# Optimization experiments

Measured on AMD Instinct MI355X. Metric: run time of the kernel, lower is better.

Reference implementation:

```python
import jax, jax.numpy as jnp
import numpy as np
from jax.scipy.linalg import expm

D = 512      # d_model
S = 3        # num_scales
BATCH = 256
H = 8        # attention heads
HD = D // H  # head dim


def layernorm(x, g, b, eps=1e-5):
    m = jnp.mean(x, axis=-1, keepdims=True)
    v = jnp.var(x, axis=-1, keepdims=True)
    return (x - m) / jnp.sqrt(v + eps) * g + b


def setup_inputs() -> dict:
    key = jax.random.key(0)
    ks = jax.random.split(key, 16)
    sd = 1.0 / np.sqrt(D)
    inp = {
        'x': jax.random.normal(ks[0], (BATCH, D), jnp.float32),
        'h_prev': jax.random.normal(ks[1], (BATCH, D), jnp.float32),
        'lstm_h': jax.random.normal(ks[2], (S, BATCH, D), jnp.float32) * 0.1,
        'lstm_c': jax.random.normal(ks[3], (S, BATCH, D), jnp.float32) * 0.1,
        'A': jax.random.normal(ks[4], (D, D), jnp.float32) * sd,
        'Bm': jax.random.normal(ks[5], (D, D), jnp.float32) * sd,
        'dn_w1': jax.random.normal(ks[6], (D, D), jnp.float32) * sd,
        'dn_b1': jnp.zeros((D,), jnp.float32),
        'dn_g': jnp.ones((D,), jnp.float32),
        'dn_beta': jnp.zeros((D,), jnp.float32),
        'dn_w2': jax.random.normal(ks[7], (1, D), jnp.float32) * sd,
        'dn_b2': jnp.zeros((1,), jnp.float32),
        'lstm_wih': jax.random.normal(ks[8], (S, 4 * D, D), jnp.float32) * sd,
        'lstm_whh': jax.random.normal(ks[9], (S, 4 * D, D), jnp.float32) * sd,
        'lstm_bih': jnp.zeros((S, 4 * D), jnp.float32),
        'lstm_bhh': jnp.zeros((S, 4 * D), jnp.float32),
        'decays': jnp.linspace(0.5, 0.95, S, dtype=jnp.float32),
        'attn_in_w': jax.random.normal(ks[10], (3 * D, D), jnp.float32) * sd,
        'attn_in_b': jnp.zeros((3 * D,), jnp.float32),
        'attn_out_w': jax.random.normal(ks[11], (D, D), jnp.float32) * sd,
        'attn_out_b': jnp.zeros((D,), jnp.float32),
        'proj_w': jax.random.normal(ks[12], (D, (S + 2) * D), jnp.float32) * (1.0 / np.sqrt((S + 2) * D)),
        'proj_b': jnp.zeros((D,), jnp.float32),
        'proj_g': jnp.ones((D,), jnp.float32),
        'proj_beta': jnp.zeros((D,), jnp.float32),
    }
    return inp


def reference(x, h_prev, lstm_h, lstm_c, A, Bm, dn_w1, dn_b1, dn_g, dn_beta,
              dn_w2, dn_b2, lstm_wih, lstm_whh, lstm_bih, lstm_bhh, decays,
              attn_in_w, attn_in_b, attn_out_w, attn_out_b,
              proj_w, proj_b, proj_g, proj_beta):
    # ---- delta_net: Linear -> LayerNorm -> GELU(exact) -> Linear -> Softplus ----
    h1 = layernorm(x @ dn_w1.T + dn_b1, dn_g, dn_beta)
    h1 = jax.nn.gelu(h1, approximate=False)
    delta = jax.nn.softplus(h1 @ dn_w2.T + dn_b2)           # (B, 1)

    # ---- SSM update: h_t = expm(delta*A) h_prev + delta*B x ----
    A_disc = jax.vmap(expm)(delta[:, :, None] * A)          # (B, D, D)
    h_ssm = jnp.einsum('bij,bj->bi', A_disc, h_prev) + delta * jnp.einsum('ij,bj->bi', Bm, x)

    # ---- multi-scale LSTM cells (vectorized over scales) ----
    gates = (jnp.einsum('bd,skd->sbk', x, lstm_wih)
             + jnp.einsum('sbd,skd->sbk', lstm_h, lstm_whh)
             + (lstm_bih + lstm_bhh)[:, None, :])           # (S, B, 4D)
    gi, gf, gg, go = jnp.split(gates, 4, axis=-1)
    i_g = jax.nn.sigmoid(gi)
    f_g = jax.nn.sigmoid(gf)
    g_g = jnp.tanh(gg)
    o_g = jax.nn.sigmoid(go)
    c_raw = f_g * lstm_c + i_g * g_g                        # (S, B, D)
    h_new = o_g * jnp.tanh(c_raw)                           # (S, B, D)
    dec = decays[:, None, None]
    c_new = dec * lstm_c + (1.0 - dec) * c_raw              # (S, B, D)

    # ---- fusion attention: 1 query (h_ssm), S keys/values (h_new) ----
    Wq, Wk, Wv = jnp.split(attn_in_w, 3, axis=0)
    bq, bk, bv = jnp.split(attn_in_b, 3, axis=0)
    kv = jnp.transpose(h_new, (1, 0, 2))                    # (B, S, D)
    q = (h_ssm @ Wq.T + bq).reshape(-1, 1, H, HD).transpose(0, 2, 1, 3)   # (B,H,1,HD)
    k = (kv @ Wk.T + bk).reshape(-1, S, H, HD).transpose(0, 2, 1, 3)      # (B,H,S,HD)
    v = (kv @ Wv.T + bv).reshape(-1, S, H, HD).transpose(0, 2, 1, 3)
    scores = jnp.einsum('bhqe,bhke->bhqk', q, k) / np.sqrt(HD)
    attn = jax.nn.softmax(scores, axis=-1)
    ctx = jnp.einsum('bhqk,bhke->bhqe', attn, v)            # (B,H,1,HD)
    ctx = ctx.transpose(0, 2, 1, 3).reshape(-1, D)          # (B, D)
    fused = ctx @ attn_out_w.T + attn_out_b                 # (B, D)

    # ---- output projection over concat [h_ssm, fused, h_1..h_S] ----
    combined = jnp.concatenate([h_ssm, fused] + [h_new[i] for i in range(S)], axis=-1)
    output = layernorm(combined @ proj_w.T + proj_b, proj_g, proj_beta)
    return (output, h_ssm, h_new, c_new)
```

## Files before the change

### kernel.cpp

```cpp
#include <hip/hip_runtime.h>
#include <math.h>

#define DIM 512
#define NB 256
#define KMAX 12

using bf16x8 = __attribute__((ext_vector_type(8))) short;
using f32x4  = __attribute__((ext_vector_type(4))) float;
using float4v = __attribute__((ext_vector_type(4))) float;
using ushort4v = __attribute__((ext_vector_type(4))) unsigned short;

__device__ __forceinline__ unsigned short f2b(float f) {
    union { float f; unsigned int u; } v; v.f = f;
    unsigned int r = v.u + 0x7fffu + ((v.u >> 16) & 1u);
    return (unsigned short)(r >> 16);
}
__device__ __forceinline__ float b2f(unsigned short u) {
    union { unsigned int u; float f; } v; v.u = ((unsigned int)u) << 16;
    return v.f;
}
__device__ __forceinline__ ushort4v f2b4(float4v v) {
    ushort4v o;
    o.x = f2b(v.x); o.y = f2b(v.y); o.z = f2b(v.z); o.w = f2b(v.w);
    return o;
}

__device__ __forceinline__ void block_reduce2(float& s, float& q, float* sb1, float* sb2)
{
    int tid = threadIdx.x;
    #pragma unroll
    for (int off = 32; off > 0; off >>= 1) {
        s += __shfl_down(s, off);
        q += __shfl_down(q, off);
    }
    if ((tid & 63) == 0) { sb1[tid >> 6] = s; sb2[tid >> 6] = q; }
    __syncthreads();
    s = sb1[0] + sb1[1] + sb1[2] + sb1[3];
    q = sb2[0] + sb2[1] + sb2[2] + sb2[3];
    __syncthreads();
}

struct GemmDesc {
    const unsigned short* X;
    const unsigned short* W;
    const float* bias;
    float* Cf;
    unsigned short* Cb;
    unsigned short* Ct;
    int M, N, K, ldX, ldW, ldC, ldCb, tr_row0, acc;
};
struct GemmArgs { GemmDesc d[8]; };
struct LnParams {
    const float* pre; const float* g; const float* beta;
    const float* w2; const float* b2; float* delta; float* coeff;
    int lnd_y;
    const float* cin; const float* bih; const float* bhh; const float* decays;
    float* hout; float* cout; unsigned short* combb;
};

__global__ __launch_bounds__(256) void gemm_mfma(GemmArgs args, LnParams lp)
{
    __shared__ unsigned short lsA[2][8192];
    __shared__ unsigned short lsB[2][8192];
    __shared__ float sb1[4], sb2[4];

    if ((int)blockIdx.y == lp.lnd_y) {
        int b = blockIdx.x, tid = threadIdx.x;
        int i0 = tid, i1 = tid + 256;
        float x0 = lp.pre[(size_t)b * DIM + i0];
        float x1 = lp.pre[(size_t)b * DIM + i1];
        float s = x0 + x1, q = x0 * x0 + x1 * x1;
        block_reduce2(s, q, sb1, sb2);
        float mean = s * (1.f / DIM);
        float var  = q * (1.f / DIM) - mean * mean;
        float inv  = rsqrtf(var + 1e-5f);
        float y0 = (x0 - mean) * inv * lp.g[i0] + lp.beta[i0];
        float y1 = (x1 - mean) * inv * lp.g[i1] + lp.beta[i1];
        float h0 = 0.5f * y0 * (1.f + erff(y0 * 0.70710678118654752f));
        float h1 = 0.5f * y1 * (1.f + erff(y1 * 0.70710678118654752f));
        float p = h0 * lp.w2[i0] + h1 * lp.w2[i1];
        float dummy = 0.f;
        block_reduce2(p, dummy, sb1, sb2);
        if (tid == 0) {
            float z = p + lp.b2[0];
            float d = (z > 20.f) ? z : log1pf(expf(z));
            lp.delta[b] = d;
            float c = 1.f;
            lp.coeff[b] = 1.f;
            for (int k = 1; k <= KMAX; ++k) { c *= d / (float)k; lp.coeff[k * 256 + b] = c; }
        }
        return;
    }

    GemmDesc de = args.d[blockIdx.y];
    int tmm = de.M >> 6;
    int tiles = tmm * (de.N >> 6);
    int t = blockIdx.x;
    if (t >= tiles) return;
    int qc = tiles >> 3, rc = tiles & 7;
    int xcd = t & 7, li = t >> 3;
    int tt = (xcd < rc) ? (xcd * (qc + 1) + li) : (rc * (qc + 1) + (xcd - rc) * qc + li);
    int m0 = (tt % tmm) << 6;
    int n0 = (tt / tmm) << 6;

    int tid = threadIdx.x;
    int w = tid >> 6;
    int l = tid & 63;
    int nkt = de.K >> 7;

    int srow = w * 16 + (l >> 2);
    int schk = l & 3;
    const unsigned short* gA = de.X + (size_t)(m0 + srow) * de.ldX + schk * 8;
    const unsigned short* gB = de.W + (size_t)(n0 + srow) * de.ldW + schk * 8;
    unsigned short* lA = &lsA[0][(w * 64 + l) * 8];
    unsigned short* lB = &lsB[0][(w * 64 + l) * 8];

#define STAGE(bufi, kt)                                                          \
    do {                                                                         \
        for (int hh = 0; hh < 4; ++hh) {                                         \
            __builtin_amdgcn_global_load_lds(                                    \
                (const __attribute__((address_space(1))) unsigned int*)(gA + (size_t)(kt) * 128 + hh * 32), \
                (__attribute__((address_space(3))) unsigned int*)(lA + (bufi) * 8192 + hh * 2048), 16, 0, 0); \
            __builtin_amdgcn_global_load_lds(                                    \
                (const __attribute__((address_space(1))) unsigned int*)(gB + (size_t)(kt) * 128 + hh * 32), \
                (__attribute__((address_space(3))) unsigned int*)(lB + (bufi) * 8192 + hh * 2048), 16, 0, 0); \
        }                                                                        \
    } while (0)

    int mbase = (w >> 1) * 32;
    int nbase = (w & 1) * 32;

    f32x4 acc[2][2];
    #pragma unroll
    for (int i = 0; i < 2; ++i)
        #pragma unroll
        for (int j = 0; j < 2; ++j)
            acc[i][j] = (f32x4){0.f, 0.f, 0.f, 0.f};

    int kg = l >> 4;
    int fr = l & 15;
    int aslot = (mbase * 4 + fr * 4 + kg) * 8;
    int bslot = (nbase * 4 + fr * 4 + kg) * 8;

    STAGE(0, 0);

    for (int kt = 0; kt < nkt; ++kt) {
        __syncthreads();
        if (kt + 1 < nkt) STAGE((kt + 1) & 1, kt + 1);

        const unsigned short* bufA = &lsA[kt & 1][0];
        const unsigned short* bufB = &lsB[kt & 1][0];
        #pragma unroll
        for (int h = 0; h < 4; ++h) {
            bf16x8 a0 = *(const bf16x8*)(bufA + h * 2048 + aslot);
            bf16x8 a1 = *(const bf16x8*)(bufA + h * 2048 + aslot + 512);
            bf16x8 b0 = *(const bf16x8*)(bufB + h * 2048 + bslot);
            bf16x8 b1 = *(const bf16x8*)(bufB + h * 2048 + bslot + 512);
            acc[0][0] = __builtin_amdgcn_mfma_f32_16x16x32_bf16(a0, b0, acc[0][0], 0, 0, 0);
            acc[0][1] = __builtin_amdgcn_mfma_f32_16x16x32_bf16(a0, b1, acc[0][1], 0, 0, 0);
            acc[1][0] = __builtin_amdgcn_mfma_f32_16x16x32_bf16(a1, b0, acc[1][0], 0, 0, 0);
            acc[1][1] = __builtin_amdgcn_mfma_f32_16x16x32_bf16(a1, b1, acc[1][1], 0, 0, 0);
        }
    }

    if (de.acc == 3) {
        __syncthreads();
        float* tile = (float*)lsA;
        #pragma unroll
        for (int mi = 0; mi < 2; ++mi)
            #pragma unroll
            for (int ni = 0; ni < 2; ++ni) {
                int ct = nbase + ni * 16 + fr;
                #pragma unroll
                for (int r = 0; r < 4; ++r) {
                    int rt = mbase + mi * 16 + kg * 4 + r;
                    tile[rt * 65 + ct] = acc[mi][ni][r];
                }
            }
        __syncthreads();
        int s = de.tr_row0;
        int d0 = n0 >> 2;
        float dec = lp.decays[s];
        for (int cell = tid; cell < 1024; cell += 256) {
            int row = cell >> 4, dsub = cell & 15;
            int d = d0 + dsub;
            int b = m0 + row;
            float vgi = tile[row * 65 +      dsub] + lp.bih[s * 2048 +        d] + lp.bhh[s * 2048 +        d];
            float vgf = tile[row * 65 + 16 + dsub] + lp.bih[s * 2048 +  512 + d] + lp.bhh[s * 2048 +  512 + d];
            float vgg = tile[row * 65 + 32 + dsub] + lp.bih[s * 2048 + 1024 + d] + lp.bhh[s * 2048 + 1024 + d];
            float vgo = tile[row * 65 + 48 + dsub] + lp.bih[s * 2048 + 1536 + d] + lp.bhh[s * 2048 + 1536 + d];
            float cc = lp.cin[(size_t)s * 131072 + (size_t)b * 512 + d];
            float ig = 1.f / (1.f + expf(-vgi));
            float fg = 1.f / (1.f + expf(-vgf));
            float g_ = tanhf(vgg);
            float og = 1.f / (1.f + expf(-vgo));
            float craw = fg * cc + ig * g_;
            float hn = og * tanhf(craw);
            lp.hout[(size_t)s * 131072 + (size_t)b * 512 + d] = hn;
            lp.cout[(size_t)s * 131072 + (size_t)b * 512 + d] = dec * cc + (1.f - dec) * craw;
            lp.combb[(size_t)b * 2048 + 512 + s * 512 + d] = f2b(hn);
        }
        return;
    }

    #pragma unroll
    for (int mi = 0; mi < 2; ++mi) {
        #pragma unroll
        for (int ni = 0; ni < 2; ++ni) {
            int col = n0 + nbase + ni * 16 + fr;
            float bv = de.bias ? de.bias[col] : 0.f;
            #pragma unroll
            for (int r = 0; r < 4; ++r) {
                int row = m0 + mbase + mi * 16 + (l >> 4) * 4 + r;
                float v = acc[mi][ni][r] + bv;
                if (de.Cf) {
                    if (de.acc == 2)      atomicAdd(&de.Cf[(size_t)row * de.ldC + col], v);
                    else if (de.acc == 1) de.Cf[(size_t)row * de.ldC + col] += v;
                    else                  de.Cf[(size_t)row * de.ldC + col] = v;
                }
                if (de.Cb)
                    de.Cb[(size_t)row * de.ldCb + col] = f2b(v);
                if (de.Ct && row >= de.tr_row0)
                    de.Ct[(size_t)col * 512 + (row - de.tr_row0)] = f2b(v);
            }
        }
    }
#undef STAGE
}

#define NSEG 13
struct PrepArgs {
    const float* sA[NSEG]; const float* sB[NSEG]; unsigned short* dst[NSEG];
    int n4[NSEG], dRL4[NSEG], sRLA4[NSEG], sRLB4[NSEG], half4[NSEG], offA[NSEG], gmap[NSEG];
    const float* A; unsigned short* ATb;
    const float* W2src; unsigned short* W2dst;
    const float* projw; const float* projb; const float* aoutb; float* pbc;
};
__global__ __launch_bounds__(256) void prep_kernel(PrepArgs a)
{
    __shared__ float tile[32][33];
    int bid = blockIdx.x, tid = threadIdx.x;
    if (bid < 2048) {
        const int gstride = 2048 * 256;
        int g0 = bid * 256 + tid;
        for (int seg = 0; seg < NSEG; ++seg) {
            int n4 = a.n4[seg];
            const float* sA = a.sA[seg];
            const float* sB = a.sB[seg];
            unsigned short* d = a.dst[seg];
            int dRL4 = a.dRL4[seg], sRLA4 = a.sRLA4[seg], sRLB4 = a.sRLB4[seg];
            int half4 = a.half4[seg], offA = a.offA[seg], gm = a.gmap[seg];
            for (int i = g0; i < n4; i += gstride) {
                int r = i / dRL4, c = i - r * dRL4;
                int rs = gm ? (((r >> 4) & 3) * 512 + ((r >> 6) << 4) + (r & 15)) : r;
                const float* src = (c < half4)
                    ? sA + ((size_t)rs * sRLA4 + offA + c) * 4
                    : sB + ((size_t)rs * sRLB4 + (c - half4)) * 4;
                float4v v = *(const float4v*)src;
                *(ushort4v*)(d + (size_t)i * 4) = f2b4(v);
            }
        }
    } else if (bid < 2560) {
        int tt = bid - 2048;
        const float* src = a.A;
        unsigned short* dst = a.ATb;
        if (tt >= 256) { tt -= 256; src = a.W2src; dst = a.W2dst; }
        int bx = tt & 15, by = tt >> 4;
        int tx = tid & 31, ty = tid >> 5;
        #pragma unroll
        for (int i = 0; i < 32; i += 8)
            tile[ty + i][tx] = src[(size_t)(by * 32 + ty + i) * 512 + bx * 32 + tx];
        __syncthreads();
        #pragma unroll
        for (int i = 0; i < 32; i += 8)
            dst[(size_t)(bx * 32 + ty + i) * 512 + by * 32 + tx] = f2b(tile[tx][ty + i]);
    } else {
        int i = (bid - 2560) * 256 + tid;
        const float* pr = a.projw + (size_t)i * 2560 + 512;
        float acc = 0.f;
        for (int j = 0; j < 512; j += 4) {
            float4v w = *(const float4v*)(pr + j);
            float4v ab = *(const float4v*)(a.aoutb + j);
            acc += w.x * ab.x + w.y * ab.y + w.z * ab.z + w.w * ab.w;
        }
        a.pbc[i] = a.projb[i] + acc;
    }
}

__global__ void pointwise_fused(
    const float* __restrict__ Tm, const float* __restrict__ coeff,
    const float* __restrict__ h_prev, const float* __restrict__ delta,
    const float* __restrict__ Bx, float* __restrict__ hssm,
    unsigned short* __restrict__ combb)
{
    int idx4 = blockIdx.x * 256 + threadIdx.x;
    int base = idx4 * 4;
    int b = base >> 9, i = base & 511;
    const float* Tr = Tm + (size_t)b * (KMAX * DIM) + i;
    float4v a = *(const float4v*)(h_prev + base);
    #pragma unroll
    for (int k = 1; k <= KMAX; ++k) {
        float c = coeff[k * 256 + b];
        float4v t = *(const float4v*)(Tr + (size_t)(k - 1) * DIM);
        a.x += c * t.x; a.y += c * t.y; a.z += c * t.z; a.w += c * t.w;
    }
    float dl = delta[b];
    float4v bx = *(const float4v*)(Bx + base);
    a.x += dl * bx.x; a.y += dl * bx.y; a.z += dl * bx.z; a.w += dl * bx.w;
    *(float4v*)(hssm + base) = a;
    *(ushort4v*)(combb + (size_t)b * 2048 + i) = f2b4(a);
}

__global__ __launch_bounds__(256) void tail_kernel(
    const unsigned short* __restrict__ qb, const unsigned short* __restrict__ kvb,
    const unsigned short* __restrict__ M2b, const float* __restrict__ projA,
    const float* __restrict__ fin_g, const float* __restrict__ fin_beta,
    float* __restrict__ outp)
{
    __shared__ float ctxs[512];
    __shared__ float sb1[4], sb2[4];
    int b = blockIdx.x, tid = threadIdx.x;

    if (tid < 128) {
        int h = tid >> 4, sub = (tid & 15) * 4;
        int col = h * 64 + sub;
        ushort4v q4 = *(const ushort4v*)(qb + (size_t)b * 512 + col);
        float qf[4] = { b2f(q4.x), b2f(q4.y), b2f(q4.z), b2f(q4.w) };
        float p[3];
        ushort4v k4[3], v4[3];
        #pragma unroll
        for (int s = 0; s < 3; ++s) {
            k4[s] = *(const ushort4v*)(kvb + (size_t)s * 262144 + (size_t)b * 1024 + col);
            v4[s] = *(const ushort4v*)(kvb + (size_t)s * 262144 + (size_t)b * 1024 + 512 + col);
            p[s] = qf[0] * b2f(k4[s].x) + qf[1] * b2f(k4[s].y)
                 + qf[2] * b2f(k4[s].z) + qf[3] * b2f(k4[s].w);
        }
        #pragma unroll
        for (int off = 1; off < 16; off <<= 1) {
            p[0] += __shfl_xor(p[0], off);
            p[1] += __shfl_xor(p[1], off);
            p[2] += __shfl_xor(p[2], off);
        }
        const float scale = 0.125f;
        float p0 = p[0] * scale, p1 = p[1] * scale, p2 = p[2] * scale;
        float m = fmaxf(p0, fmaxf(p1, p2));
        float w0 = expf(p0 - m), w1 = expf(p1 - m), w2 = expf(p2 - m);
        float invs = 1.f / (w0 + w1 + w2);
        ctxs[col + 0] = (w0 * b2f(v4[0].x) + w1 * b2f(v4[1].x) + w2 * b2f(v4[2].x)) * invs;
        ctxs[col + 1] = (w0 * b2f(v4[0].y) + w1 * b2f(v4[1].y) + w2 * b2f(v4[2].y)) * invs;
        ctxs[col + 2] = (w0 * b2f(v4[0].z) + w1 * b2f(v4[1].z) + w2 * b2f(v4[2].z)) * invs;
        ctxs[col + 3] = (w0 * b2f(v4[0].w) + w1 * b2f(v4[1].w) + w2 * b2f(v4[2].w)) * invs;
    }
    __syncthreads();

    float x0 = projA[(size_t)b * 512 + tid];
    float x1 = projA[(size_t)b * 512 + tid + 256];
    {
        const unsigned short* mr0 = M2b + (size_t)tid * 512;
        const unsigned short* mr1 = M2b + (size_t)(tid + 256) * 512;
        for (int k = 0; k < 512; k += 8) {
            ushort4v a0 = *(const ushort4v*)(mr0 + k);
            ushort4v a1 = *(const ushort4v*)(mr0 + k + 4);
            ushort4v c0 = *(const ushort4v*)(mr1 + k);
            ushort4v c1 = *(const ushort4v*)(mr1 + k + 4);
            float t0 = ctxs[k+0], t1 = ctxs[k+1], t2 = ctxs[k+2], t3 = ctxs[k+3];
            float t4 = ctxs[k+4], t5 = ctxs[k+5], t6 = ctxs[k+6], t7 = ctxs[k+7];
            x0 += t0*b2f(a0.x) + t1*b2f(a0.y) + t2*b2f(a0.z) + t3*b2f(a0.w)
                + t4*b2f(a1.x) + t5*b2f(a1.y) + t6*b2f(a1.z) + t7*b2f(a1.w);
            x1 += t0*b2f(c0.x) + t1*b2f(c0.y) + t2*b2f(c0.z) + t3*b2f(c0.w)
                + t4*b2f(c1.x) + t5*b2f(c1.y) + t6*b2f(c1.z) + t7*b2f(c1.w);
        }
    }

    float s = x0 + x1, q = x0 * x0 + x1 * x1;
    block_reduce2(s, q, sb1, sb2);
    float mean = s * (1.f / DIM);
    float var  = q * (1.f / DIM) - mean * mean;
    float inv  = rsqrtf(var + 1e-5f);
    outp[(size_t)b * DIM + tid]       = (x0 - mean) * inv * fin_g[tid]       + fin_beta[tid];
    outp[(size_t)b * DIM + tid + 256] = (x1 - mean) * inv * fin_g[tid + 256] + fin_beta[tid + 256];
}

extern "C" void kernel_launch(void* const* d_in, const int* in_sizes, int n_in,
                              void* d_out, int out_size, void* d_ws, size_t ws_size,
                              hipStream_t stream)
{
    const float* x        = (const float*)d_in[0];
    const float* h_prev   = (const float*)d_in[1];
    const float* lstm_h   = (const float*)d_in[2];
    const float* lstm_c   = (const float*)d_in[3];
    const float* A        = (const float*)d_in[4];
    const float* Bm       = (const float*)d_in[5];
    const float* dn_w1    = (const float*)d_in[6];
    const float* dn_b1    = (const float*)d_in[7];
    const float* dn_g     = (const float*)d_in[8];
    const float* dn_beta  = (const float*)d_in[9];
    const float* dn_w2    = (const float*)d_in[10];
    const float* dn_b2    = (const float*)d_in[11];
    const float* wih      = (const float*)d_in[12];
    const float* whh      = (const float*)d_in[13];
    const float* bih      = (const float*)d_in[14];
    const float* bhh      = (const float*)d_in[15];
    const float* decays   = (const float*)d_in[16];
    const float* ain_w    = (const float*)d_in[17];
    const float* ain_b    = (const float*)d_in[18];
    const float* aout_w   = (const float*)d_in[19];
    const float* aout_b   = (const float*)d_in[20];
    const float* proj_w   = (const float*)d_in[21];
    const float* proj_b   = (const float*)d_in[22];
    const float* proj_g   = (const float*)d_in[23];
    const float* proj_bt  = (const float*)d_in[24];

    float* out  = (float*)d_out;
    float* hssm = out + 131072;
    float* hnew = out + 262144;
    float* cnew = out + 655360;

    unsigned short* us = (unsigned short*)d_ws;
    unsigned short* hpb     = us;
    unsigned short* ATb     = us + 131072;
    unsigned short* dn_w1b  = us + 393216;
    unsigned short* Bmb     = us + 655360;
    unsigned short* ain_wb  = us + 917504;
    unsigned short* proj_wb = us + 1703936;
    unsigned short* P2b     = us + 2752512;
    unsigned short* aout_wTb= us + 3014656;
    unsigned short* Pw      = us + 3276800;
    unsigned short* Qa      = us + 5373952;
    unsigned short* Qb      = us + 5636096;
    unsigned short* Wcat    = us + 5898240;
    unsigned short* Xcat    = us + 12189696;
    unsigned short* combb   = us + 12976128;
    unsigned short* qb      = us + 13500416;
    unsigned short* kvb     = us + 13631488;
    unsigned short* Tmb     = us + 14417920;
    float* fbase  = (float*)(us + 14942208);
    float* pre1   = fbase;
    float* delta  = fbase + 131072;
    float* coeff  = fbase + 131328;
    float* Bx     = fbase + 134656;
    float* Tm     = fbase + 265728;
    float* pbc    = fbase + 1838592;
    unsigned short* M2b = (unsigned short*)(fbase + 1839104);
    float* projout = pre1;

    LnParams lpOff;
    lpOff.pre = nullptr; lpOff.g = nullptr; lpOff.beta = nullptr;
    lpOff.w2 = nullptr; lpOff.b2 = nullptr; lpOff.delta = nullptr; lpOff.coeff = nullptr;
    lpOff.lnd_y = -1;
    lpOff.cin = lstm_c; lpOff.bih = bih; lpOff.bhh = bhh; lpOff.decays = decays;
    lpOff.hout = hnew; lpOff.cout = cnew; lpOff.combb = combb;

    PrepArgs pa;
    int sidx = 0;
    auto LIN = [&](const float* s, unsigned short* d, int n4) {
        pa.sA[sidx]=s; pa.sB[sidx]=s; pa.dst[sidx]=d; pa.n4[sidx]=n4;
        pa.dRL4[sidx]=n4; pa.sRLA4[sidx]=0; pa.sRLB4[sidx]=0;
        pa.half4[sidx]=n4; pa.offA[sidx]=0; pa.gmap[sidx]=0; ++sidx;
    };
    LIN(h_prev, hpb,     32768);
    LIN(A,      Pw,      65536);
    LIN(dn_w1,  dn_w1b,  65536);
    LIN(Bm,     Bmb,     65536);
    LIN(ain_w,  ain_wb,  196608);
    pa.sA[sidx]=proj_w; pa.sB[sidx]=proj_w + 1024; pa.dst[sidx]=proj_wb; pa.n4[sidx]=262144;
    pa.dRL4[sidx]=512; pa.sRLA4[sidx]=640; pa.sRLB4[sidx]=640; pa.half4[sidx]=128; pa.offA[sidx]=0; pa.gmap[sidx]=0; ++sidx;
    pa.sA[sidx]=proj_w; pa.sB[sidx]=proj_w; pa.dst[sidx]=P2b; pa.n4[sidx]=65536;
    pa.dRL4[sidx]=128; pa.sRLA4[sidx]=640; pa.sRLB4[sidx]=640; pa.half4[sidx]=128; pa.offA[sidx]=128; pa.gmap[sidx]=0; ++sidx;
    for (int s = 0; s < 3; ++s) {
        pa.sA[sidx]=wih + (size_t)s*1048576; pa.sB[sidx]=whh + (size_t)s*1048576;
        pa.dst[sidx]=Wcat + (size_t)s*2097152; pa.n4[sidx]=524288;
        pa.dRL4[sidx]=256; pa.sRLA4[sidx]=128; pa.sRLB4[sidx]=128; pa.half4[sidx]=128; pa.offA[sidx]=0;
        pa.gmap[sidx]=1; ++sidx;
    }
    for (int s = 0; s < 3; ++s) {
        pa.sA[sidx]=x; pa.sB[sidx]=lstm_h + (size_t)s*131072;
        pa.dst[sidx]=Xcat + (size_t)s*262144; pa.n4[sidx]=65536;
        pa.dRL4[sidx]=256; pa.sRLA4[sidx]=128; pa.sRLB4[sidx]=128; pa.half4[sidx]=128; pa.offA[sidx]=0;
        pa.gmap[sidx]=0; ++sidx;
    }
    pa.A = A; pa.ATb = ATb;
    pa.W2src = aout_w; pa.W2dst = aout_wTb;
    pa.projw = proj_w; pa.projb = proj_b; pa.aoutb = aout_b; pa.pbc = pbc;
    prep_kernel<<<2562, 256, 0, stream>>>(pa);

    GemmArgs ga;
    ga.d[0] = { Xcat, dn_w1b, dn_b1, pre1, nullptr, nullptr, 256, 512, 512, 1024, 512, 512, 0, 0, 0 };
    ga.d[1] = { Xcat, Bmb,    nullptr, Bx,  nullptr, nullptr, 256, 512, 512, 1024, 512, 512, 0, 0, 0 };
    ga.d[2] = { Pw, ATb, nullptr, nullptr, Pw + 1*262144, Qa, 512, 512, 512, 512, 512, 512, 512, 0, 0 };
    for (int s = 0; s < 3; ++s)
        ga.d[3 + s] = { Xcat + (size_t)s * 262144, Wcat + (size_t)s * 2097152, nullptr,
                        nullptr, nullptr, nullptr,
                        256, 2048, 1024, 1024, 1024, 2048, 0, s, 3 };
    ga.d[6] = { P2b, aout_wTb, nullptr, nullptr, M2b, nullptr, 512, 512, 512, 512, 512, 512, 512, 0, 0 };
    ga.d[7] = { hpb, Pw, nullptr, Tm, Tmb, nullptr, 256, 512, 512, 512, 512, 6144, 2048, 0, 0 };
    gemm_mfma<<<dim3(128, 8), 256, 0, stream>>>(ga, lpOff);

    LnParams lp1 = lpOff;
    lp1.pre = pre1; lp1.g = dn_g; lp1.beta = dn_beta; lp1.w2 = dn_w2; lp1.b2 = dn_b2;
    lp1.delta = delta; lp1.coeff = coeff; lp1.lnd_y = 3;
    ga.d[0] = { Pw + 1*262144, Qa, nullptr, nullptr, Pw + 3*262144, Qb, 512, 512, 512, 512, 512, 512, 512, 0, 0 };
    ga.d[1] = { hpb, Pw + 1*262144, nullptr, Tm + 512,  Tmb + 512,  nullptr, 256, 512, 512, 512,  512, 6144, 2048, 0, 0 };
    ga.d[2] = { Tmb, Pw + 1*262144, nullptr, Tm + 1024, Tmb + 1024, nullptr, 256, 512, 512, 2048, 512, 6144, 2048, 0, 0 };
    gemm_mfma<<<dim3(256, 4), 256, 0, stream>>>(ga, lp1);

    ga.d[0] = { Pw + 3*262144, Qb, nullptr, nullptr, Pw + 7*262144, nullptr, 512, 512, 512, 512, 512, 512, 512, 0, 0 };
    ga.d[1] = { hpb,        Pw + 3*262144, nullptr, Tm + 1536, Tmb + 1536, nullptr, 256, 512, 512, 512,  512, 6144, 2048, 0, 0 };
    ga.d[2] = { Tmb,        Pw + 3*262144, nullptr, Tm + 2048, nullptr, nullptr, 256, 512, 512, 2048, 512, 6144, 0, 0, 0 };
    ga.d[3] = { Tmb + 512,  Pw + 3*262144, nullptr, Tm + 2560, nullptr, nullptr, 256, 512, 512, 2048, 512, 6144, 0, 0, 0 };
    ga.d[4] = { Tmb + 1024, Pw + 3*262144, nullptr, Tm + 3072, nullptr, nullptr, 256, 512, 512, 2048, 512, 6144, 0, 0, 0 };
    gemm_mfma<<<dim3(64, 5), 256, 0, stream>>>(ga, lpOff);

    ga.d[0] = { Tmb + 1536, Pw + 3*262144, nullptr, Tm + 3584, nullptr, nullptr, 256, 512, 512, 2048, 512, 6144, 0, 0, 0 };
    ga.d[1] = { Tmb,        Pw + 7*262144, nullptr, Tm + 4096, nullptr, nullptr, 256, 512, 512, 2048, 512, 6144, 0, 0, 0 };
    ga.d[2] = { Tmb + 512,  Pw + 7*262144, nullptr, Tm + 4608, nullptr, nullptr, 256, 512, 512, 2048, 512, 6144, 0, 0, 0 };
    ga.d[3] = { Tmb + 1024, Pw + 7*262144, nullptr, Tm + 5120, nullptr, nullptr, 256, 512, 512, 2048, 512, 6144, 0, 0, 0 };
    ga.d[4] = { Tmb + 1536, Pw + 7*262144, nullptr, Tm + 5632, nullptr, nullptr, 256, 512, 512, 2048, 512, 6144, 0, 0, 0 };
    gemm_mfma<<<dim3(32, 5), 256, 0, stream>>>(ga, lpOff);

    pointwise_fused<<<128, 256, 0, stream>>>(Tm, coeff, h_prev, delta, Bx, hssm, combb);

    ga.d[0] = { combb, ain_wb, ain_b, nullptr, qb, nullptr, 256, 512, 512, 2048, 512, 512, 512, 0, 0 };
    for (int s = 0; s < 3; ++s)
        ga.d[1 + s] = { combb + 512 + (size_t)s * 512, ain_wb + 262144, ain_b + 512,
                        nullptr, kvb + (size_t)s * 262144, nullptr, 256, 1024, 512, 2048, 512, 1024, 1024, 0, 0 };
    ga.d[4] = { combb, proj_wb, pbc, projout, nullptr, nullptr, 256, 512, 2048, 2048, 2048, 512, 0, 0, 0 };
    gemm_mfma<<<dim3(64, 5), 256, 0, stream>>>(ga, lpOff);

    tail_kernel<<<256, 256, 0, stream>>>(qb, kvb, M2b, projout,
                                         proj_g, proj_bt, out);
}
```

Before: 225.1 us.

## Read fp32 weights directly in GEMM staging instead of pre-converting to bf16

Removes the prep-kernel conversion of dn_w1, Bm, LSTM weights, attention in-proj and projection weights to bf16 copies. The GEMM instead loads those weights as fp32 from global memory, converts them to bf16 in registers and writes them to LDS, with the LSTM row-gather remap moved into the load. This saves one full read-write pass over the large weight set. In exchange the B operand is loaded synchronously rather than through async global-to-LDS copies, and weights read by several tiles are converted repeatedly.

Result: slower. 247.7 us (+10.1%).

```diff
diff --git a/kernel.cpp b/kernel.cpp
--- a/kernel.cpp
+++ b/kernel.cpp
@@ -43,11 +43,14 @@
 struct GemmDesc {
     const unsigned short* X;
     const unsigned short* W;
+    const float* Wf;
+    const float* Wf2;
     const float* bias;
     float* Cf;
     unsigned short* Cb;
     unsigned short* Ct;
     int M, N, K, ldX, ldW, ldC, ldCb, tr_row0, acc;
+    int wmode, ldWf, wsplit, gmapf;
 };
 struct GemmArgs { GemmDesc d[8]; };
 struct LnParams {
@@ -115,15 +118,32 @@
     unsigned short* lA = &lsA[0][(w * 64 + l) * 8];
     unsigned short* lB = &lsB[0][(w * 64 + l) * 8];
 
+    int wrow = n0 + srow;
+    int wsr = wrow;
+    if (de.wmode && de.gmapf)
+        wsr = ((wrow >> 4) & 3) * 512 + ((wrow >> 6) << 4) + (wrow & 15);
+
 #define STAGE(bufi, kt)                                                          \
     do {                                                                         \
         for (int hh = 0; hh < 4; ++hh) {                                         \
             __builtin_amdgcn_global_load_lds(                                    \
                 (const __attribute__((address_space(1))) unsigned int*)(gA + (size_t)(kt) * 128 + hh * 32), \
                 (__attribute__((address_space(3))) unsigned int*)(lA + (bufi) * 8192 + hh * 2048), 16, 0, 0); \
-            __builtin_amdgcn_global_load_lds(                                    \
-                (const __attribute__((address_space(1))) unsigned int*)(gB + (size_t)(kt) * 128 + hh * 32), \
-                (__attribute__((address_space(3))) unsigned int*)(lB + (bufi) * 8192 + hh * 2048), 16, 0, 0); \
+            if (de.wmode == 0) {                                                 \
+                __builtin_amdgcn_global_load_lds(                                \
+                    (const __attribute__((address_space(1))) unsigned int*)(gB + (size_t)(kt) * 128 + hh * 32), \
+                    (__attribute__((address_space(3))) unsigned int*)(lB + (bufi) * 8192 + hh * 2048), 16, 0, 0); \
+            } else {                                                             \
+                int c = (kt) * 128 + hh * 32 + schk * 8;                         \
+                const float* ws = (c < de.wsplit)                                \
+                    ? de.Wf  + (size_t)wsr * de.ldWf + c                         \
+                    : de.Wf2 + (size_t)wsr * de.ldWf + (c - de.wsplit);          \
+                float4v w0 = *(const float4v*)ws;                                \
+                float4v w1 = *(const float4v*)(ws + 4);                          \
+                unsigned short* ld = lB + (bufi) * 8192 + hh * 2048;             \
+                *(ushort4v*)ld       = f2b4(w0);                                 \
+                *(ushort4v*)(ld + 4) = f2b4(w1);                                 \
+            }                                                                    \
         }                                                                        \
     } while (0)
 
@@ -228,10 +248,10 @@
 #undef STAGE
 }
 
-#define NSEG 13
+#define NSEG 6
 struct PrepArgs {
     const float* sA[NSEG]; const float* sB[NSEG]; unsigned short* dst[NSEG];
-    int n4[NSEG], dRL4[NSEG], sRLA4[NSEG], sRLB4[NSEG], half4[NSEG], offA[NSEG], gmap[NSEG];
+    int n4[NSEG], dRL4[NSEG], sRLA4[NSEG], sRLB4[NSEG], half4[NSEG], offA[NSEG];
     const float* A; unsigned short* ATb;
     const float* W2src; unsigned short* W2dst;
     const float* projw; const float* projb; const float* aoutb; float* pbc;
@@ -240,8 +260,8 @@
 {
     __shared__ float tile[32][33];
     int bid = blockIdx.x, tid = threadIdx.x;
-    if (bid < 2048) {
-        const int gstride = 2048 * 256;
+    if (bid < 512) {
+        const int gstride = 512 * 256;
         int g0 = bid * 256 + tid;
         for (int seg = 0; seg < NSEG; ++seg) {
             int n4 = a.n4[seg];
@@ -249,19 +269,18 @@
             const float* sB = a.sB[seg];
             unsigned short* d = a.dst[seg];
             int dRL4 = a.dRL4[seg], sRLA4 = a.sRLA4[seg], sRLB4 = a.sRLB4[seg];
-            int half4 = a.half4[seg], offA = a.offA[seg], gm = a.gmap[seg];
+            int half4 = a.half4[seg], offA = a.offA[seg];
             for (int i = g0; i < n4; i += gstride) {
                 int r = i / dRL4, c = i - r * dRL4;
-                int rs = gm ? (((r >> 4) & 3) * 512 + ((r >> 6) << 4) + (r & 15)) : r;
                 const float* src = (c < half4)
-                    ? sA + ((size_t)rs * sRLA4 + offA + c) * 4
-                    : sB + ((size_t)rs * sRLB4 + (c - half4)) * 4;
+                    ? sA + ((size_t)r * sRLA4 + offA + c) * 4
+                    : sB + ((size_t)r * sRLB4 + (c - half4)) * 4;
                 float4v v = *(const float4v*)src;
                 *(ushort4v*)(d + (size_t)i * 4) = f2b4(v);
             }
         }
-    } else if (bid < 2560) {
-        int tt = bid - 2048;
+    } else if (bid < 1024) {
+        int tt = bid - 512;
         const float* src = a.A;
         unsigned short* dst = a.ATb;
         if (tt >= 256) { tt -= 256; src = a.W2src; dst = a.W2dst; }
@@ -275,7 +294,7 @@
         for (int i = 0; i < 32; i += 8)
             dst[(size_t)(bx * 32 + ty + i) * 512 + by * 32 + tx] = f2b(tile[tx][ty + i]);
     } else {
-        int i = (bid - 2560) * 256 + tid;
+        int i = (bid - 1024) * 256 + tid;
         const float* pr = a.projw + (size_t)i * 2560 + 512;
         float acc = 0.f;
         for (int j = 0; j < 512; j += 4) {
@@ -419,16 +438,11 @@
     unsigned short* us = (unsigned short*)d_ws;
     unsigned short* hpb     = us;
     unsigned short* ATb     = us + 131072;
-    unsigned short* dn_w1b  = us + 393216;
-    unsigned short* Bmb     = us + 655360;
-    unsigned short* ain_wb  = us + 917504;
-    unsigned short* proj_wb = us + 1703936;
     unsigned short* P2b     = us + 2752512;
     unsigned short* aout_wTb= us + 3014656;
     unsigned short* Pw      = us + 3276800;
     unsigned short* Qa      = us + 5373952;
     unsigned short* Qb      = us + 5636096;
-    unsigned short* Wcat    = us + 5898240;
     unsigned short* Xcat    = us + 12189696;
     unsigned short* combb   = us + 12976128;
     unsigned short* qb      = us + 13500416;
@@ -444,6 +458,25 @@
     unsigned short* M2b = (unsigned short*)(fbase + 1839104);
     float* projout = pre1;
 
+    auto B16 = [](const unsigned short* X, const unsigned short* W, const float* bias,
+                  float* Cf, unsigned short* Cb, unsigned short* Ct,
+                  int M, int N, int K, int ldX, int ldW, int ldC, int ldCb,
+                  int tr0, int acc) {
+        GemmDesc d{}; d.X = X; d.W = W; d.bias = bias; d.Cf = Cf; d.Cb = Cb; d.Ct = Ct;
+        d.M = M; d.N = N; d.K = K; d.ldX = ldX; d.ldW = ldW; d.ldC = ldC; d.ldCb = ldCb;
+        d.tr_row0 = tr0; d.acc = acc; d.wmode = 0; return d;
+    };
+    auto F32W = [](const unsigned short* X, const float* Wf, const float* Wf2,
+                   int ldWf, int wsplit, int gmapf, const float* bias,
+                   float* Cf, unsigned short* Cb, unsigned short* Ct,
+                   int M, int N, int K, int ldX, int ldC, int ldCb,
+                   int tr0, int acc) {
+        GemmDesc d{}; d.X = X; d.Wf = Wf; d.Wf2 = Wf2; d.ldWf = ldWf;
+        d.wsplit = wsplit; d.gmapf = gmapf; d.bias = bias; d.Cf = Cf; d.Cb = Cb; d.Ct = Ct;
+        d.M = M; d.N = N; d.K = K; d.ldX = ldX; d.ldC = ldC; d.ldCb = ldCb;
+        d.tr_row0 = tr0; d.acc = acc; d.wmode = 1; return d;
+    };
+
     LnParams lpOff;
     lpOff.pre = nullptr; lpOff.g = nullptr; lpOff.beta = nullptr;
     lpOff.w2 = nullptr; lpOff.b2 = nullptr; lpOff.delta = nullptr; lpOff.coeff = nullptr;
@@ -456,75 +489,87 @@
     auto LIN = [&](const float* s, unsigned short* d, int n4) {
         pa.sA[sidx]=s; pa.sB[sidx]=s; pa.dst[sidx]=d; pa.n4[sidx]=n4;
         pa.dRL4[sidx]=n4; pa.sRLA4[sidx]=0; pa.sRLB4[sidx]=0;
-        pa.half4[sidx]=n4; pa.offA[sidx]=0; pa.gmap[sidx]=0; ++sidx;
+        pa.half4[sidx]=n4; pa.offA[sidx]=0; ++sidx;
     };
     LIN(h_prev, hpb,     32768);
     LIN(A,      Pw,      65536);
-    LIN(dn_w1,  dn_w1b,  65536);
-    LIN(Bm,     Bmb,     65536);
-    LIN(ain_w,  ain_wb,  196608);
-    pa.sA[sidx]=proj_w; pa.sB[sidx]=proj_w + 1024; pa.dst[sidx]=proj_wb; pa.n4[sidx]=262144;
-    pa.dRL4[sidx]=512; pa.sRLA4[sidx]=640; pa.sRLB4[sidx]=640; pa.half4[sidx]=128; pa.offA[sidx]=0; pa.gmap[sidx]=0; ++sidx;
     pa.sA[sidx]=proj_w; pa.sB[sidx]=proj_w; pa.dst[sidx]=P2b; pa.n4[sidx]=65536;
-    pa.dRL4[sidx]=128; pa.sRLA4[sidx]=640; pa.sRLB4[sidx]=640; pa.half4[sidx]=128; pa.offA[sidx]=128; pa.gmap[sidx]=0; ++sidx;
-    for (int s = 0; s < 3; ++s) {
-        pa.sA[sidx]=wih + (size_t)s*1048576; pa.sB[sidx]=whh + (size_t)s*1048576;
-        pa.dst[sidx]=Wcat + (size_t)s*2097152; pa.n4[sidx]=524288;
-        pa.dRL4[sidx]=256; pa.sRLA4[sidx]=128; pa.sRLB4[sidx]=128; pa.half4[sidx]=128; pa.offA[sidx]=0;
-        pa.gmap[sidx]=1; ++sidx;
-    }
+    pa.dRL4[sidx]=128; pa.sRLA4[sidx]=640; pa.sRLB4[sidx]=640; pa.half4[sidx]=128; pa.offA[sidx]=128; ++sidx;
     for (int s = 0; s < 3; ++s) {
         pa.sA[sidx]=x; pa.sB[sidx]=lstm_h + (size_t)s*131072;
         pa.dst[sidx]=Xcat + (size_t)s*262144; pa.n4[sidx]=65536;
-        pa.dRL4[sidx]=256; pa.sRLA4[sidx]=128; pa.sRLB4[sidx]=128; pa.half4[sidx]=128; pa.offA[sidx]=0;
-        pa.gmap[sidx]=0; ++sidx;
+        pa.dRL4[sidx]=256; pa.sRLA4[sidx]=128; pa.sRLB4[sidx]=128; pa.half4[sidx]=128; pa.offA[sidx]=0; ++sidx;
     }
     pa.A = A; pa.ATb = ATb;
     pa.W2src = aout_w; pa.W2dst = aout_wTb;
     pa.projw = proj_w; pa.projb = proj_b; pa.aoutb = aout_b; pa.pbc = pbc;
-    prep_kernel<<<2562, 256, 0, stream>>>(pa);
+    prep_kernel<<<1026, 256, 0, stream>>>(pa);
 
     GemmArgs ga;
-    ga.d[0] = { Xcat, dn_w1b, dn_b1, pre1, nullptr, nullptr, 256, 512, 512, 1024, 512, 512, 0, 0, 0 };
-    ga.d[1] = { Xcat, Bmb,    nullptr, Bx,  nullptr, nullptr, 256, 512, 512, 1024, 512, 512, 0, 0, 0 };
-    ga.d[2] = { Pw, ATb, nullptr, nullptr, Pw + 1*262144, Qa, 512, 512, 512, 512, 512, 512, 512, 0, 0 };
+    ga.d[0] = F32W(Xcat, dn_w1, dn_w1, 512, 512, 0, dn_b1, pre1, nullptr, nullptr,
+                   256, 512, 512, 1024, 512, 0, 0, 0);
+    ga.d[1] = F32W(Xcat, Bm, Bm, 512, 512, 0, nullptr, Bx, nullptr, nullptr,
+                   256, 512, 512, 1024, 512, 0, 0, 0);
+    ga.d[2] = B16(Pw, ATb, nullptr, nullptr, Pw + 1*262144, Qa,
+                  512, 512, 512, 512, 512, 512, 512, 0, 0);
     for (int s = 0; s < 3; ++s)
-        ga.d[3 + s] = { Xcat + (size_t)s * 262144, Wcat + (size_t)s * 2097152, nullptr,
-                        nullptr, nullptr, nullptr,
-                        256, 2048, 1024, 1024, 1024, 2048, 0, s, 3 };
-    ga.d[6] = { P2b, aout_wTb, nullptr, nullptr, M2b, nullptr, 512, 512, 512, 512, 512, 512, 512, 0, 0 };
-    ga.d[7] = { hpb, Pw, nullptr, Tm, Tmb, nullptr, 256, 512, 512, 512, 512, 6144, 2048, 0, 0 };
+        ga.d[3 + s] = F32W(Xcat + (size_t)s * 262144,
+                           wih + (size_t)s * 1048576, whh + (size_t)s * 1048576,
+                           512, 512, 1, nullptr, nullptr, nullptr, nullptr,
+                           256, 2048, 1024, 1024, 0, 0, s, 3);
+    ga.d[6] = B16(P2b, aout_wTb, nullptr, nullptr, M2b, nullptr,
+                  512, 512, 512, 512, 512, 512, 512, 0, 0);
+    ga.d[7] = B16(hpb, Pw, nullptr, Tm, Tmb, nullptr,
+                  256, 512, 512, 512, 512, 6144, 2048, 0, 0);
     gemm_mfma<<<dim3(128, 8), 256, 0, stream>>>(ga, lpOff);
 
     LnParams lp1 = lpOff;
     lp1.pre = pre1; lp1.g = dn_g; lp1.beta = dn_beta; lp1.w2 = dn_w2; lp1.b2 = dn_b2;
     lp1.delta = delta; lp1.coeff = coeff; lp1.lnd_y = 3;
-    ga.d[0] = { Pw + 1*262144, Qa, nullptr, nullptr, Pw + 3*262144, Qb, 512, 512, 512, 512, 512, 512, 512, 0, 0 };
-    ga.d[1] = { hpb, Pw + 1*262144, nullptr, Tm + 512,  Tmb + 512,  nullptr, 256, 512, 512, 512,  512, 6144, 2048, 0, 0 };
-    ga.d[2] = { Tmb, Pw + 1*262144, nullptr, Tm + 1024, Tmb + 1024, nullptr, 256, 512, 512, 2048, 512, 6144, 2048, 0, 0 };
+    ga.d[0] = B16(Pw + 1*262144, Qa, nullptr, nullptr, Pw + 3*262144, Qb,
+                  512, 512, 512, 512, 512, 512, 512, 0, 0);
+    ga.d[1] = B16(hpb, Pw + 1*262144, nullptr, Tm + 512,  Tmb + 512,  nullptr,
+                  256, 512, 512, 512,  512, 6144, 2048, 0, 0);
+    ga.d[2] = B16(Tmb, Pw + 1*262144, nullptr, Tm + 1024, Tmb + 1024, nullptr,
+                  256, 512, 512, 2048, 512, 6144, 2048, 0, 0);
     gemm_mfma<<<dim3(256, 4), 256, 0, stream>>>(ga, lp1);
 
-    ga.d[0] = { Pw + 3*262144, Qb, nullptr, nullptr, Pw + 7*262144, nullptr, 512, 512, 512, 512, 512, 512, 512, 0, 0 };
-    ga.d[1] = { hpb,        Pw + 3*262144, nullptr, Tm + 1536, Tmb + 1536, nullptr, 256, 512, 512, 512,  512, 6144, 2048, 0, 0 };
-    ga.d[2] = { Tmb,        Pw + 3*262144, nullptr, Tm + 2048, nullptr, nullptr, 256, 512, 512, 2048, 512, 6144, 0, 0, 0 };
-    ga.d[3] = { Tmb + 512,  Pw + 3*262144, nullptr, Tm + 2560, nullptr, nullptr, 256, 512, 512, 2048, 512, 6144, 0, 0, 0 };
-    ga.d[4] = { Tmb + 1024, Pw + 3*262144, nullptr, Tm + 3072, nullptr, nullptr, 256, 512, 512, 2048, 512, 6144, 0, 0, 0 };
+    ga.d[0] = B16(Pw + 3*262144, Qb, nullptr, nullptr, Pw + 7*262144, nullptr,
+                  512, 512, 512, 512, 512, 512, 512, 0, 0);
+    ga.d[1] = B16(hpb,        Pw + 3*262144, nullptr, Tm + 1536, Tmb + 1536, nullptr,
+                  256, 512, 512, 512,  512, 6144, 2048, 0, 0);
+    ga.d[2] = B16(Tmb,        Pw + 3*262144, nullptr, Tm + 2048, nullptr, nullptr,
+                  256, 512, 512, 2048, 512, 6144, 0, 0, 0);
+    ga.d[3] = B16(Tmb + 512,  Pw + 3*262144, nullptr, Tm + 2560, nullptr, nullptr,
+                  256, 512, 512, 2048, 512, 6144, 0, 0, 0);
+    ga.d[4] = B16(Tmb + 1024, Pw + 3*262144, nullptr, Tm + 3072, nullptr, nullptr,
+                  256, 512, 512, 2048, 512, 6144, 0, 0, 0);
     gemm_mfma<<<dim3(64, 5), 256, 0, stream>>>(ga, lpOff);
 
-    ga.d[0] = { Tmb + 1536, Pw + 3*262144, nullptr, Tm + 3584, nullptr, nullptr, 256, 512, 512, 2048, 512, 6144, 0, 0, 0 };
-    ga.d[1] = { Tmb,        Pw + 7*262144, nullptr, Tm + 4096, nullptr, nullptr, 256, 512, 512, 2048, 512, 6144, 0, 0, 0 };
-    ga.d[2] = { Tmb + 512,  Pw + 7*262144, nullptr, Tm + 4608, nullptr, nullptr, 256, 512, 512, 2048, 512, 6144, 0, 0, 0 };
-    ga.d[3] = { Tmb + 1024, Pw + 7*262144, nullptr, Tm + 5120, nullptr, nullptr, 256, 512, 512, 2048, 512, 6144, 0, 0, 0 };
-    ga.d[4] = { Tmb + 1536, Pw + 7*262144, nullptr, Tm + 5632, nullptr, nullptr, 256, 512, 512, 2048, 512, 6144, 0, 0, 0 };
+    ga.d[0] = B16(Tmb + 1536, Pw + 3*262144, nullptr, Tm + 3584, nullptr, nullptr,
+                  256, 512, 512, 2048, 512, 6144, 0, 0, 0);
+    ga.d[1] = B16(Tmb,        Pw + 7*262144, nullptr, Tm + 4096, nullptr, nullptr,
+                  256, 512, 512, 2048, 512, 6144, 0, 0, 0);
+    ga.d[2] = B16(Tmb + 512,  Pw + 7*262144, nullptr, Tm + 4608, nullptr, nullptr,
+                  256, 512, 512, 2048, 512, 6144, 0, 0, 0);
+    ga.d[3] = B16(Tmb + 1024, Pw + 7*262144, nullptr, Tm + 5120, nullptr, nullptr,
+                  256, 512, 512, 2048, 512, 6144, 0, 0, 0);
+    ga.d[4] = B16(Tmb + 1536, Pw + 7*262144, nullptr, Tm + 5632, nullptr, nullptr,
+                  256, 512, 512, 2048, 512, 6144, 0, 0, 0);
     gemm_mfma<<<dim3(32, 5), 256, 0, stream>>>(ga, lpOff);
 
     pointwise_fused<<<128, 256, 0, stream>>>(Tm, coeff, h_prev, delta, Bx, hssm, combb);
 
-    ga.d[0] = { combb, ain_wb, ain_b, nullptr, qb, nullptr, 256, 512, 512, 2048, 512, 512, 512, 0, 0 };
+    ga.d[0] = F32W(combb, ain_w, ain_w, 512, 512, 0, ain_b, nullptr, qb, nullptr,
+                   256, 512, 512, 2048, 0, 512, 0, 0);
     for (int s = 0; s < 3; ++s)
-        ga.d[1 + s] = { combb + 512 + (size_t)s * 512, ain_wb + 262144, ain_b + 512,
-                        nullptr, kvb + (size_t)s * 262144, nullptr, 256, 1024, 512, 2048, 512, 1024, 1024, 0, 0 };
-    ga.d[4] = { combb, proj_wb, pbc, projout, nullptr, nullptr, 256, 512, 2048, 2048, 2048, 512, 0, 0, 0 };
+        ga.d[1 + s] = F32W(combb + 512 + (size_t)s * 512,
+                           ain_w + 262144, ain_w + 262144, 512, 1024, 0, ain_b + 512,
+                           nullptr, kvb + (size_t)s * 262144, nullptr,
+                           256, 1024, 512, 2048, 0, 1024, 0, 0);
+    ga.d[4] = F32W(combb, proj_w, proj_w + 1024, 2560, 512, 0, pbc,
+                   projout, nullptr, nullptr,
+                   256, 512, 2048, 2048, 512, 0, 0, 0);
     gemm_mfma<<<dim3(64, 5), 256, 0, stream>>>(ga, lpOff);
 
     tail_kernel<<<256, 256, 0, stream>>>(qb, kvb, M2b, projout,
```
